# Performance work log

Measured on AMD Instinct MI355X. Metric: run time of the kernel, lower is better.

## Reference

```python
import jax, jax.numpy as jnp
import numpy as np

B, C, N, L, K, PRED = 64, 2, 1024, 24, 3, 12


def setup_inputs() -> dict:
    key = jax.random.key(0)
    ks = jax.random.split(key, 32)
    u = lambda k, shape, s: jax.random.uniform(k, shape, jnp.float32, -s, s)
    stdv_gc = 1.0 / np.sqrt(N)
    stdv_g = 1.0 / np.sqrt(N * (K + 1))
    stdv_r = 1.0 / np.sqrt(2 * N)
    inp = {
        'inputs': jax.random.normal(ks[0], (B, C, N, L), jnp.float32),
        'adj': (jax.random.uniform(ks[1], (N, N)) < 0.05).astype(jnp.float32),
        'gc_w': u(ks[2], (K, N, N), stdv_gc),
        'Wf': u(ks[3], (N, N * (K + 1)), stdv_g), 'bf': u(ks[4], (N,), stdv_g),
        'Wi': u(ks[5], (N, N * (K + 1)), stdv_g), 'bi': u(ks[6], (N,), stdv_g),
        'Wo': u(ks[7], (N, N * (K + 1)), stdv_g), 'bo': u(ks[8], (N,), stdv_g),
        'Wc': u(ks[9], (N, N * (K + 1)), stdv_g), 'bc': u(ks[10], (N,), stdv_g),
        'rWf': u(ks[11], (N, 2 * N), stdv_r), 'rbf': u(ks[12], (N,), stdv_r),
        'rWi': u(ks[13], (N, 2 * N), stdv_r), 'rbi': u(ks[14], (N,), stdv_r),
        'rWo': u(ks[15], (N, 2 * N), stdv_r), 'rbo': u(ks[16], (N,), stdv_r),
        'rWc': u(ks[17], (N, 2 * N), stdv_r), 'rbc': u(ks[18], (N,), stdv_r),
        'neighbor_w': u(ks[19], (N,), stdv_gc),
        'c': jnp.ones((1,), jnp.float32),
        'conv_w': u(ks[20], (C * PRED, C), 1.0 / np.sqrt(C)),
        'conv_b': u(ks[21], (C * PRED,), 1.0 / np.sqrt(C)),
    }
    return inp


def _build_A_list(adj, k):
    # tmp = sum(A, 0); zeros -> 1e-5; 'D_inverse' = diag(tmp) (as in original code)
    tmp = jnp.sum(adj, 0)
    tmp = jnp.where(tmp == 0, 1e-5, tmp)
    a_norm = tmp[:, None] * adj  # diag(tmp) @ A
    a_list = []
    a_tmp = jnp.eye(adj.shape[0], dtype=adj.dtype)
    for _ in range(k):
        a_tmp = jnp.minimum(a_tmp @ a_norm, 1.0)  # clamp max=1.0
        a_list.append(a_tmp)
    return a_list


def _forward(adj, inputs, gc_w, Wf, bf, Wi, bi, Wo, bo, Wc, bc,
             rWf, rbf, rWi, rbi, rWo, rbo, rWc, rbc, neighbor_w, c, conv_w, conv_b):
    b, ch, n, l = inputs.shape
    k = gc_w.shape[0]
    a_list = _build_A_list(adj, k)
    a_stack = jnp.stack(a_list)            # (K,N,N)
    eff_w = a_stack * gc_w                 # masked FilterLinear weights
    nbr = a_list[-1] @ neighbor_w          # (N,)
    Wg = jnp.concatenate([Wf, Wi, Wo, Wc], 0)      # fused gate weights (4N, (K+1)N)
    bg = jnp.concatenate([bf, bi, bo, bc], 0)
    rWg = jnp.concatenate([rWf, rWi, rWo, rWc], 0)  # (4N, 2N)
    rbg = jnp.concatenate([rbf, rbi, rbo, rbc], 0)

    def step(carry, x):  # x: (B,C,N)
        H, Cs, rH, rCs, _ = carry
        # gc = cat_k FilterLinear_k(x), each x @ (A_k*W_k)^T
        gc = jnp.einsum('bcn,kmn->bckm', x, eff_w).reshape(b, ch, k * n)
        g = jnp.concatenate([gc, H], -1) @ Wg.T + bg
        f, i, o, Ct = jnp.split(g, 4, -1)
        Cs = jax.nn.sigmoid(f) * (Cs * nbr) + jax.nn.sigmoid(i) * jnp.tanh(Ct)
        H = jax.nn.sigmoid(o) * jnp.tanh(Cs)
        rg = jnp.concatenate([x, rH], -1) @ rWg.T + rbg
        rf, ri, ro, rCt = jnp.split(rg, 4, -1)
        rCs = jax.nn.sigmoid(rf) * rCs + jax.nn.sigmoid(ri) * jnp.tanh(rCt)
        rH = jax.nn.sigmoid(ro) * jnp.tanh(rCs)
        var1 = jnp.var(x, axis=(0, 2), keepdims=True, ddof=1)   # (1,C,1), unbiased like torch
        var2 = jnp.var(gc, axis=(0, 2), keepdims=True, ddof=1)
        pred = (H * var1 * c + rH * var2) / (var1 + var2 * c)
        return (H, Cs, rH, rCs, pred), None

    z = jnp.zeros((b, ch, n), inputs.dtype)
    xs = jnp.moveaxis(inputs, -1, 0)  # (L,B,C,N)
    (H, Cs, rH, rCs, pred), _ = jax.lax.scan(step, (z, z, z, z, z), xs)
    # Conv1d(C, C*pred_len, k=1) then reshape (B,C,N,pred_len)
    out = jnp.einsum('bcn,oc->bon', pred, conv_w) + conv_b[:, None]
    return out.reshape(b, ch, n, -1)


def reference(inputs, adj, gc_w, Wf, bf, Wi, bi, Wo, bo, Wc, bc,
              rWf, rbf, rWi, rbi, rWo, rbo, rWc, rbc, neighbor_w, c, conv_w, conv_b):
    return _forward(adj, inputs, gc_w, Wf, bf, Wi, bi, Wo, bo, Wc, bc,
                    rWf, rbf, rWi, rbi, rWo, rbo, rWc, rbc, neighbor_w, c, conv_w, conv_b)
```

## Files before the change

### kernel.cpp

```cpp
#include <hip/hip_runtime.h>
#include <cmath>

#define NN 1024
#define BC 128
#define LS 24

typedef unsigned short u16;
typedef __attribute__((ext_vector_type(4))) float f32x4;
typedef __attribute__((ext_vector_type(8))) short bf16x8;
typedef __attribute__((ext_vector_type(8))) unsigned short u16x8;

typedef __attribute__((address_space(1))) const void* as1cv;
typedef __attribute__((address_space(3))) void* as3v;

#define GLD16(gp, lp) __builtin_amdgcn_global_load_lds((as1cv)(gp), (as3v)(lp), 16, 0, 0)

__device__ __forceinline__ float sigf(float x){ return 1.0f/(1.0f+expf(-x)); }

__device__ __forceinline__ u16 f2b(float x){
  union { float f; unsigned u; } v; v.f = x;
  unsigned r = v.u + 0x7FFFu + ((v.u >> 16) & 1u);
  return (u16)(r >> 16);
}
__device__ __forceinline__ float b2f(u16 b){
  union { unsigned u; float f; } v; v.u = ((unsigned)b) << 16;
  return v.f;
}

__global__ void k_prep(const float* __restrict__ inputs, const float* __restrict__ adj,
                       const float* __restrict__ Wf, const float* __restrict__ Wi,
                       const float* __restrict__ Wo, const float* __restrict__ Wc,
                       const float* __restrict__ rWf, const float* __restrict__ rWi,
                       const float* __restrict__ rWo, const float* __restrict__ rWc,
                       const float* __restrict__ bf_, const float* __restrict__ bi_,
                       const float* __restrict__ bo_, const float* __restrict__ bc_,
                       const float* __restrict__ rbf, const float* __restrict__ rbi,
                       const float* __restrict__ rbo, const float* __restrict__ rbc,
                       u16* __restrict__ Xb, float* __restrict__ csum,
                       u16* __restrict__ Wgxb, u16* __restrict__ WgHp,
                       u16* __restrict__ rWgxb, u16* __restrict__ rWgHp,
                       float* __restrict__ bgcat){
  int b = blockIdx.x, tid = threadIdx.x;
  if (b < 512){
    int idx = b*256 + tid;
    const float4* p = (const float4*)(inputs + (size_t)idx*LS);
    float v[LS];
    #pragma unroll
    for (int q = 0; q < 6; ++q){
      float4 f = p[q];
      v[q*4]=f.x; v[q*4+1]=f.y; v[q*4+2]=f.z; v[q*4+3]=f.w;
    }
    #pragma unroll
    for (int t = 0; t < LS; ++t)
      Xb[(size_t)t*BC*NN + idx] = f2b(v[t]);
  } else if (b < 576){
    int bb = b - 512;
    for (int j = tid; j < 1024; j += 256){
      float s = 0.f;
      for (int i = 0; i < 16; ++i) s += adj[(size_t)(bb*16+i)*1024 + j];
      csum[(size_t)bb*1024 + j] = s;
    }
  } else if (b < 592){
    int idx = (b-576)*256 + tid;
    int seg = idx >> 10, j = idx & 1023;
    bgcat[idx]      = (seg==0?bf_: seg==1?bi_: seg==2?bo_:bc_)[j];
    bgcat[4096+idx] = (seg==0?rbf: seg==1?rbi: seg==2?rbo:rbc)[j];
  } else {
    int idx = (b-592)*256 + tid;
    if (idx < 2097152){
      int kg = idx & 511, r = idx >> 9;
      int seg = r >> 10, j = r & 1023;
      const float* W = (seg==0?Wf: seg==1?Wi: seg==2?Wo:Wc) + (size_t)j*4096 + kg*8;
      float4 a = *(const float4*)W;
      float4 c = *(const float4*)(W + 4);
      u16x8 o = { f2b(a.x), f2b(a.y), f2b(a.z), f2b(a.w),
                  f2b(c.x), f2b(c.y), f2b(c.z), f2b(c.w) };
      if (kg < 384) *(u16x8*)(Wgxb + (size_t)r*3072 + kg*8) = o;
      else {
        int p = (j>>3)*32 + seg*8 + (j&7);
        *(u16x8*)(WgHp + (size_t)p*1024 + (kg*8 - 3072)) = o;
      }
    } else {
      int g2 = idx - 2097152;
      int kg = g2 & 255, r = g2 >> 8;
      int seg = r >> 10, j = r & 1023;
      const float* W = (seg==0?rWf: seg==1?rWi: seg==2?rWo:rWc) + (size_t)j*2048 + kg*8;
      float4 a = *(const float4*)W;
      float4 c = *(const float4*)(W + 4);
      u16x8 o = { f2b(a.x), f2b(a.y), f2b(a.z), f2b(a.w),
                  f2b(c.x), f2b(c.y), f2b(c.z), f2b(c.w) };
      if (kg < 128) *(u16x8*)(rWgxb + (size_t)r*1024 + kg*8) = o;
      else {
        int p = (j>>3)*32 + seg*8 + (j&7);
        *(u16x8*)(rWgHp + (size_t)p*1024 + (kg*8 - 1024)) = o;
      }
    }
  }
}

__global__ void k_colsum2(const float* __restrict__ part, float* __restrict__ tmp){
  int j = blockIdx.x*256 + threadIdx.x;
  float s = 0.f;
  for (int b = 0; b < 64; ++b) s += part[(size_t)b*1024 + j];
  tmp[j] = (s == 0.f) ? 1e-5f : s;
}

__global__ void k_anormT(const float* __restrict__ adj, const float* __restrict__ tmp,
                         u16* __restrict__ A1b, u16* __restrict__ anormT){
  __shared__ u16 t[64][65];
  int bi = blockIdx.y*64, bj = blockIdx.x*64;
  for (int e = threadIdx.x; e < 4096; e += 256){
    int r = e >> 6, cc = e & 63;
    float v = tmp[bi+r]*adj[(size_t)(bi+r)*1024 + bj+cc];
    A1b[(size_t)(bi+r)*1024 + bj+cc] = f2b(fminf(v, 1.f));
    t[r][cc] = f2b(v);
  }
  __syncthreads();
  for (int e = threadIdx.x; e < 4096; e += 256){
    int r = e >> 6, cc = e & 63;
    anormT[(size_t)(bj+r)*1024 + bi+cc] = t[cc][r];
  }
}

__global__ void k_nbr(const u16* __restrict__ A3b, const float* __restrict__ nw,
                      float* __restrict__ nbr){
  __shared__ float red[256];
  int row = blockIdx.x;
  float s = 0.f;
  for (int j = threadIdx.x; j < 1024; j += 256)
    s += b2f(A3b[(size_t)row*1024 + j])*nw[j];
  red[threadIdx.x] = s; __syncthreads();
  for (int st = 128; st > 0; st >>= 1){
    if (threadIdx.x < st) red[threadIdx.x] += red[threadIdx.x+st];
    __syncthreads();
  }
  if (threadIdx.x == 0) nbr[row] = red[0];
}

__global__ void k_effT(const u16* __restrict__ Ap, const float* __restrict__ gcw,
                       u16* __restrict__ effb, u16* __restrict__ effbT){
  __shared__ u16 t[64][65];
  int bi = blockIdx.y*64, bj = blockIdx.x*64;
  for (int e = threadIdx.x; e < 4096; e += 256){
    int r = e >> 6, cc = e & 63;
    size_t idx = (size_t)(bi+r)*1024 + bj+cc;
    u16 v = f2b(b2f(Ap[idx]) * gcw[idx]);
    effb[idx] = v;
    t[r][cc] = v;
  }
  __syncthreads();
  for (int e = threadIdx.x; e < 4096; e += 256){
    int r = e >> 6, cc = e & 63;
    effbT[(size_t)(bj+r)*3072 + bi+cc] = t[cc][r];
  }
}

__device__ __forceinline__ void mfma_tile(
    const u16* __restrict__ A, const u16* __restrict__ Bw, int K,
    const float* __restrict__ bias,
    float* __restrict__ outf, u16* __restrict__ outb, int ldc,
    u16* ldsA, u16* ldsB)
{
  const int tid  = threadIdx.x;
  const int lane = tid & 63;
  const int w    = tid >> 6;
  const int wr   = (w >> 1) * 64;
  const int wc   = (w & 1) * 64;
  f32x4 acc[4][4] = {};

  const int lrow = lane >> 3;
  const int srck = ((lane & 7) ^ lrow) * 8;
  for (int k0 = 0; k0 < K; k0 += 64){
    #pragma unroll
    for (int c = 0; c < 4; ++c){
      int row = w*32 + c*8;
      GLD16(A  + (size_t)(row + lrow)*K + k0 + srck, &ldsA[row*64]);
      GLD16(Bw + (size_t)(row + lrow)*K + k0 + srck, &ldsB[row*64]);
    }
    __syncthreads();
    #pragma unroll
    for (int kk = 0; kk < 2; ++kk) {
      bf16x8 af[4], bfr[4];
      #pragma unroll
      for (int mi = 0; mi < 4; ++mi) {
        int row = wr + mi*16 + (lane & 15);
        int grp = (kk*4 + (lane >> 4)) ^ (row & 7);
        af[mi] = *(const bf16x8*)&ldsA[row*64 + grp*8];
      }
      #pragma unroll
      for (int ni = 0; ni < 4; ++ni) {
        int row = wc + ni*16 + (lane & 15);
        int grp = (kk*4 + (lane >> 4)) ^ (row & 7);
        bfr[ni] = *(const bf16x8*)&ldsB[row*64 + grp*8];
      }
      #pragma unroll
      for (int mi = 0; mi < 4; ++mi)
        #pragma unroll
        for (int ni = 0; ni < 4; ++ni)
          acc[mi][ni] = __builtin_amdgcn_mfma_f32_16x16x32_bf16(af[mi], bfr[ni], acc[mi][ni], 0, 0, 0);
    }
    __syncthreads();
  }
  #pragma unroll
  for (int mi = 0; mi < 4; ++mi) {
    #pragma unroll
    for (int ni = 0; ni < 4; ++ni) {
      int col = wc + ni*16 + (lane & 15);
      #pragma unroll
      for (int q = 0; q < 4; ++q) {
        int row = wr + mi*16 + (lane >> 4)*4 + q;
        float v = acc[mi][ni][q];
        if (bias) v += bias[col];
        if (outf) outf[(size_t)row*ldc + col] = v;
        if (outb) outb[(size_t)row*ldc + col] = f2b(v);
      }
    }
  }
}

__global__ __launch_bounds__(256) void k_mfma_pre(
    const u16* __restrict__ Xb, const u16* __restrict__ Bcat,
    const float* __restrict__ bgcat, u16* __restrict__ prebuf)
{
  __shared__ u16 lds[16384];
  int id = blockIdx.y*64 + blockIdx.x;
  int bx = (id & 7)*8 + ((id >> 3) & 7);
  int by = id >> 6;
  mfma_tile(Xb + (size_t)by*128*1024, Bcat + (size_t)bx*128*1024, 1024,
            bgcat + bx*128, nullptr,
            prebuf + (size_t)by*128*8192 + bx*128, 8192,
            lds, lds + 8192);
}

__global__ __launch_bounds__(256) void k_mfma64(
    const u16* __restrict__ Ag, const u16* __restrict__ Bg, int K,
    int clamp1, int swz, u16* __restrict__ outb, int ldc)
{
  __shared__ u16 ldsA[64*128];
  __shared__ u16 ldsB[64*128];
  const int tid  = threadIdx.x;
  const int lane = tid & 63;
  const int w    = tid >> 6;
  const int wr   = (w >> 1) * 32;
  const int wc   = (w & 1) * 32;
  int bx = blockIdx.x, by = blockIdx.y;
  if (swz){
    int id = by*16 + bx;
    by = (id & 7)*8 + ((id >> 3) & 7);
    bx = id >> 6;
  }
  const u16* A = Ag + (size_t)by*64*K;
  const u16* B = Bg + (size_t)bx*64*K;
  f32x4 acc[2][2] = {};

  const int r4  = lane >> 4;
  const int g16 = lane & 15;
  for (int k0 = 0; k0 < K; k0 += 128){
    #pragma unroll
    for (int c = 0; c < 4; ++c){
      int rowb = w*16 + c*4;
      int row = rowb + r4;
      int srcg = (g16 & 8) | ((g16 & 7) ^ (row & 7));
      GLD16(A + (size_t)row*K + k0 + srcg*8, &ldsA[rowb*128]);
      GLD16(B + (size_t)row*K + k0 + srcg*8, &ldsB[rowb*128]);
    }
    __syncthreads();
    #pragma unroll
    for (int kk = 0; kk < 4; ++kk){
      int idx = kk*4 + (lane >> 4);
      bf16x8 af[2], bfr[2];
      #pragma unroll
      for (int mi = 0; mi < 2; ++mi){
        int row = wr + mi*16 + (lane & 15);
        int pa = (idx & 8) | ((idx & 7) ^ (row & 7));
        af[mi] = *(const bf16x8*)&ldsA[row*128 + pa*8];
      }
      #pragma unroll
      for (int ni = 0; ni < 2; ++ni){
        int row = wc + ni*16 + (lane & 15);
        int pb = (idx & 8) | ((idx & 7) ^ (row & 7));
        bfr[ni] = *(const bf16x8*)&ldsB[row*128 + pb*8];
      }
      #pragma unroll
      for (int mi = 0; mi < 2; ++mi)
        #pragma unroll
        for (int ni = 0; ni < 2; ++ni)
          acc[mi][ni] = __builtin_amdgcn_mfma_f32_16x16x32_bf16(af[mi], bfr[ni], acc[mi][ni], 0, 0, 0);
    }
    __syncthreads();
  }
  #pragma unroll
  for (int mi = 0; mi < 2; ++mi){
    #pragma unroll
    for (int ni = 0; ni < 2; ++ni){
      int col = bx*64 + wc + ni*16 + (lane & 15);
      #pragma unroll
      for (int q = 0; q < 4; ++q){
        int row = by*64 + wr + mi*16 + (lane >> 4)*4 + q;
        float v = acc[mi][ni][q];
        if (clamp1) v = fminf(v, 1.f);
        outb[(size_t)row*ldc + col] = f2b(v);
      }
    }
  }
}

__global__ __launch_bounds__(256) void k_step(
    const u16* __restrict__ WgHp, const u16* __restrict__ rWgHp,
    const u16* __restrict__ pre_t,
    const float* __restrict__ nbrv,
    u16* __restrict__ Hb2, u16* __restrict__ rHb2,
    float* __restrict__ Cs, float* __restrict__ rCs,
    float* __restrict__ Hf, float* __restrict__ rHf,
    int ph, int last)
{
  __shared__ u16 ldsA[64*256];
  __shared__ u16 ldsB[32*256];

  const int tid  = threadIdx.x;
  const int lane = tid & 63;
  const int w    = tid >> 6;
  const int bid  = blockIdx.x;
  const int job  = bid >> 8;
  const int rem  = bid & 255;
  const int s    = rem >> 1;
  const int r0   = (rem & 1) * 64;

  const u16* Bp   = (job ? rWgHp : WgHp) + (size_t)s*32*1024;
  const u16* Ab   = (job ? rHb2 : Hb2) + (size_t)ph*BC*NN + (size_t)r0*NN;
  const u16* pret = pre_t + (size_t)job*4096;
  u16* Hnext  = (job ? rHb2 : Hb2) + (size_t)(ph^1)*BC*NN;
  float* Csb  = job ? rCs : Cs;
  float* Hfin = job ? rHf : Hf;

  const int g32   = lane & 31;
  const int rhalf = lane >> 5;

  f32x4 acc[2] = {};
  for (int t = 0; t < 4; ++t){
    int k0 = t*256;
    #pragma unroll
    for (int c = 0; c < 8; ++c){
      int rowb = w*16 + c*2;
      int row = rowb + rhalf;
      int srcg = (g32 & 24) | ((g32 & 7) ^ (row & 7));
      GLD16(Ab + (size_t)row*1024 + k0 + srcg*8, &ldsA[rowb*256]);
    }
    #pragma unroll
    for (int c = 0; c < 4; ++c){
      int rowb = w*8 + c*2;
      int row = rowb + rhalf;
      int srcg = (g32 & 24) | ((g32 & 7) ^ (row & 7));
      GLD16(Bp + (size_t)row*1024 + k0 + srcg*8, &ldsB[rowb*256]);
    }
    __syncthreads();
    #pragma unroll
    for (int kk = 0; kk < 8; ++kk){
      int idx = kk*4 + (lane >> 4);
      int rowa = w*16 + (lane & 15);
      int pa = (idx & 24) | ((idx & 7) ^ (rowa & 7));
      bf16x8 af = *(const bf16x8*)&ldsA[rowa*256 + pa*8];
      #pragma unroll
      for (int ni = 0; ni < 2; ++ni){
        int rowb2 = ni*16 + (lane & 15);
        int pb = (idx & 24) | ((idx & 7) ^ (rowb2 & 7));
        bf16x8 bv = *(const bf16x8*)&ldsB[rowb2*256 + pb*8];
        acc[ni] = __builtin_amdgcn_mfma_f32_16x16x32_bf16(af, bv, acc[ni], 0, 0, 0);
      }
    }
    __syncthreads();
  }

  #pragma unroll
  for (int ni = 0; ni < 2; ++ni){
    int pcol = ni*16 + (lane & 15);
    int gcol = (pcol >> 3)*1024 + s*8 + (pcol & 7);
    #pragma unroll
    for (int q = 0; q < 4; ++q){
      int row = r0 + w*16 + (lane >> 4)*4 + q;
      acc[ni][q] += b2f(pret[(size_t)row*8192 + gcol]);
    }
  }
  const bool act = (lane & 15) < 8;
  const int  c   = lane & 7;
  const int  col = s*8 + c;
  float fac = 1.f;
  if (!job && act) fac = nbrv[col];
  #pragma unroll
  for (int q = 0; q < 4; ++q){
    float a0 = acc[0][q], a1 = acc[1][q];
    float p1 = __shfl_xor(a0, 8);
    float p3 = __shfl_xor(a1, 8);
    if (act){
      int row = r0 + w*16 + (lane >> 4)*4 + q;
      float fg = sigf(a0), ig = sigf(p1), og = sigf(a1), ct = tanhf(p3);
      size_t cidx = (size_t)row*NN + col;
      float cs = fg*Csb[cidx]*fac + ig*ct;
      Csb[cidx] = cs;
      float h = og*tanhf(cs);
      Hnext[cidx] = f2b(h);
      if (last) Hfin[cidx] = h;
    }
  }
}

__global__ void k_var1(const u16* __restrict__ Xl, const u16* __restrict__ gcl,
                       float* __restrict__ part){
  int ch = blockIdx.x & 1, seg = blockIdx.x >> 1;
  int tid = threadIdx.x;
  float s1=0.f,q1=0.f,s2=0.f,q2=0.f;
  for (int bb = 0; bb < 2; ++bb){
    int row = (seg*2+bb)*2 + ch;
    const u16* xr = Xl + (size_t)row*1024;
    for (int n = tid; n < 1024; n += 256){ float v = b2f(xr[n]); s1 += v; q1 += v*v; }
    const u16* gr = gcl + (size_t)row*3072;
    for (int n = tid; n < 3072; n += 256){ float v = b2f(gr[n]); s2 += v; q2 += v*v; }
  }
  __shared__ float red[256][4];
  red[tid][0]=s1; red[tid][1]=q1; red[tid][2]=s2; red[tid][3]=q2;
  __syncthreads();
  for (int st = 128; st > 0; st >>= 1){
    if (tid < st){ for (int z = 0; z < 4; ++z) red[tid][z] += red[tid+st][z]; }
    __syncthreads();
  }
  if (tid == 0){ for (int z = 0; z < 4; ++z) part[(size_t)blockIdx.x*4 + z] = red[0][z]; }
}

__global__ void k_out(const float* __restrict__ H, const float* __restrict__ rH,
                      const float* __restrict__ part, const float* __restrict__ cptr,
                      const float* __restrict__ cw, const float* __restrict__ cb,
                      float* __restrict__ out){
  __shared__ float vsh[4];
  int tid = threadIdx.x;
  if (tid < 4){
    int ch = tid & 1, which = tid >> 1;
    float s = 0.f, q = 0.f;
    for (int seg = 0; seg < 32; ++seg){
      const float* p = part + (size_t)(seg*2+ch)*4 + which*2;
      s += p[0]; q += p[1];
    }
    float n = which ? 196608.f : 65536.f;
    vsh[tid] = (q - s*s/n) / (n - 1.f);
  }
  __syncthreads();
  int idx = blockIdx.x*256 + tid;
  int n = idx & 1023, b = idx >> 10;
  float c0 = cptr[0];
  float v10 = vsh[0], v11 = vsh[1], v20 = vsh[2], v21 = vsh[3];
  size_t i0 = (size_t)(b*2+0)*1024 + n, i1 = (size_t)(b*2+1)*1024 + n;
  float p0 = (H[i0]*v10*c0 + rH[i0]*v20) / (v10 + v20*c0);
  float p1 = (H[i1]*v11*c0 + rH[i1]*v21) / (v11 + v21*c0);
  float* ob = out + (size_t)b*24*1024 + n;
  #pragma unroll
  for (int o = 0; o < 24; ++o)
    ob[(size_t)o*1024] = p0*cw[o*2+0] + p1*cw[o*2+1] + cb[o];
}

extern "C" void kernel_launch(void* const* d_in, const int* in_sizes, int n_in,
                              void* d_out, int out_size, void* d_ws, size_t ws_size,
                              hipStream_t stream) {
  const float* inputs = (const float*)d_in[0];
  const float* adj    = (const float*)d_in[1];
  const float* gcw    = (const float*)d_in[2];
  const float* Wf  = (const float*)d_in[3];  const float* bf_ = (const float*)d_in[4];
  const float* Wi  = (const float*)d_in[5];  const float* bi_ = (const float*)d_in[6];
  const float* Wo  = (const float*)d_in[7];  const float* bo_ = (const float*)d_in[8];
  const float* Wc  = (const float*)d_in[9];  const float* bc_ = (const float*)d_in[10];
  const float* rWf = (const float*)d_in[11]; const float* rbf = (const float*)d_in[12];
  const float* rWi = (const float*)d_in[13]; const float* rbi = (const float*)d_in[14];
  const float* rWo = (const float*)d_in[15]; const float* rbo = (const float*)d_in[16];
  const float* rWc = (const float*)d_in[17]; const float* rbc = (const float*)d_in[18];
  const float* nw     = (const float*)d_in[19];
  const float* cscal  = (const float*)d_in[20];
  const float* convw  = (const float*)d_in[21];
  const float* convb  = (const float*)d_in[22];
  float* out = (float*)d_out;

  char* cur = (char*)d_ws;
  auto alloc = [&](size_t bytes) -> void* {
    void* p = cur; cur += (bytes + 255) & ~(size_t)255; return p;
  };
  u16*   Xb     = (u16*)  alloc((size_t)LS*BC*NN*2);
  float* csum   = (float*)alloc((size_t)64*1024*4);
  float* tmpv   = (float*)alloc(1024*4);
  u16*   anormT = (u16*)  alloc((size_t)NN*NN*2);
  u16*   Apowb  = (u16*)  alloc((size_t)3*NN*NN*2);
  float* nbrv   = (float*)alloc(1024*4);
  u16*   effb   = (u16*)  alloc((size_t)3*NN*NN*2);
  u16*   effbT  = (u16*)  alloc((size_t)3*NN*NN*2);
  u16*   Wgxb   = (u16*)  alloc((size_t)4096*3072*2);
  u16*   WgHp   = (u16*)  alloc((size_t)4096*1024*2);
  u16*   rWgHp  = (u16*)  alloc((size_t)4096*1024*2);
  u16*   Bcat   = (u16*)  alloc((size_t)8192*1024*2);
  float* bgcat  = (float*)alloc(8192*4);
  u16*   gclb   = (u16*)  alloc((size_t)BC*3072*2);
  u16*   prebuf = (u16*)  alloc((size_t)3072*8192*2);
  char*  zbase  = cur;
  u16*   Hb2    = (u16*)  alloc((size_t)2*BC*NN*2);
  u16*   rHb2   = (u16*)  alloc((size_t)2*BC*NN*2);
  float* Cs     = (float*)alloc((size_t)BC*NN*4);
  float* rCs    = (float*)alloc((size_t)BC*NN*4);
  size_t zlen   = (size_t)(cur - zbase);
  float* Hfv    = (float*)alloc((size_t)BC*NN*4);
  float* rHfv   = (float*)alloc((size_t)BC*NN*4);
  float* part   = (float*)alloc(64*4*4);

  u16* A1b = Apowb;
  u16* A2b = Apowb + (size_t)NN*NN;
  u16* A3b = Apowb + (size_t)2*NN*NN;
  u16* Cwb   = Bcat;
  u16* rWgxb = Bcat + (size_t)4096*1024;

  k_prep<<<592 + (2097152+1048576)/256, 256, 0, stream>>>(
      inputs, adj, Wf, Wi, Wo, Wc, rWf, rWi, rWo, rWc,
      bf_, bi_, bo_, bc_, rbf, rbi, rbo, rbc,
      Xb, csum, Wgxb, WgHp, rWgxb, rWgHp, bgcat);
  k_colsum2<<<4, 256, 0, stream>>>(csum, tmpv);
  dim3 g16(16, 16);
  k_anormT<<<g16, 256, 0, stream>>>(adj, tmpv, A1b, anormT);
  k_mfma64<<<g16, 256, 0, stream>>>(A1b, anormT, 1024, 1, 0, A2b, 1024);
  k_mfma64<<<g16, 256, 0, stream>>>(A2b, anormT, 1024, 1, 0, A3b, 1024);
  k_nbr<<<NN, 256, 0, stream>>>(A3b, nw, nbrv);
  dim3 geff(16, 48);
  k_effT<<<geff, 256, 0, stream>>>(Apowb, gcw, effb, effbT);

  dim3 gcwg(16, 64);
  k_mfma64<<<gcwg, 256, 0, stream>>>(Wgxb, effbT, 3072, 0, 1, Cwb, 1024);
  dim3 gpre(64, 24);
  k_mfma_pre<<<gpre, 256, 0, stream>>>(Xb, Bcat, bgcat, prebuf);
  dim3 ggcl(48, 2);
  k_mfma64<<<ggcl, 256, 0, stream>>>(Xb + (size_t)(LS-1)*BC*NN, effb, 1024, 0, 0, gclb, 3072);

  hipMemsetAsync(zbase, 0, zlen, stream);

  for (int t = 0; t < LS; ++t)
    k_step<<<512, 256, 0, stream>>>(WgHp, rWgHp,
        prebuf + (size_t)t*BC*8192,
        nbrv, Hb2, rHb2, Cs, rCs, Hfv, rHfv, t & 1, t == LS-1);

  k_var1<<<64, 256, 0, stream>>>(Xb + (size_t)(LS-1)*BC*NN, gclb, part);
  k_out<<<(64*1024)/256, 256, 0, stream>>>(Hfv, rHfv, part, cscal, convw, convb, out);
}
```

Baseline: 529.6 us.

## Double-buffer LDS staging in recurrent step GEMM to overlap loads with MFMA

The k_step recurrent GEMM now splits K into 8 chunks of 128 with two LDS buffers, issuing global-to-LDS loads for the next chunk before computing the current one. It uses explicit vmcnt waits and raw s_barrier in place of __syncthreads. The goal is to hide global load latency behind MFMA work in this latency-bound per-timestep kernel. The cost is more barriers per chunk and reliance on hand-counted vmcnt values, which could break if the compiler changes how many loads it emits.

```diff
diff --git a/kernel.cpp b/kernel.cpp
--- a/kernel.cpp
+++ b/kernel.cpp
@@ -314,8 +314,8 @@
     float* __restrict__ Hf, float* __restrict__ rHf,
     int ph, int last)
 {
-  __shared__ u16 ldsA[64*256];
-  __shared__ u16 ldsB[32*256];
+  __shared__ u16 ldsA[2][64*128];
+  __shared__ u16 ldsB[2][32*128];
 
   const int tid  = threadIdx.x;
   const int lane = tid & 63;
@@ -333,42 +333,56 @@
   float* Csb  = job ? rCs : Cs;
   float* Hfin = job ? rHf : Hf;
 
-  const int g32   = lane & 31;
-  const int rhalf = lane >> 5;
+  const int r4  = lane >> 4;
+  const int g16 = lane & 15;
+
+  auto STAGE = [&](int ck, int buf){
+    int k0 = ck*128;
+    #pragma unroll
+    for (int c = 0; c < 4; ++c){
+      int rowb = w*16 + c*4;
+      int row = rowb + r4;
+      int srcg = (g16 & 8) | ((g16 & 7) ^ (row & 7));
+      GLD16(Ab + (size_t)row*1024 + k0 + srcg*8, &ldsA[buf][rowb*128]);
+    }
+    #pragma unroll
+    for (int c = 0; c < 2; ++c){
+      int rowb = w*8 + c*4;
+      int row = rowb + r4;
+      int srcg = (g16 & 8) | ((g16 & 7) ^ (row & 7));
+      GLD16(Bp + (size_t)row*1024 + k0 + srcg*8, &ldsB[buf][rowb*128]);
+    }
+  };
 
   f32x4 acc[2] = {};
-  for (int t = 0; t < 4; ++t){
-    int k0 = t*256;
-    #pragma unroll
-    for (int c = 0; c < 8; ++c){
-      int rowb = w*16 + c*2;
-      int row = rowb + rhalf;
-      int srcg = (g32 & 24) | ((g32 & 7) ^ (row & 7));
-      GLD16(Ab + (size_t)row*1024 + k0 + srcg*8, &ldsA[rowb*256]);
-    }
-    #pragma unroll
-    for (int c = 0; c < 4; ++c){
-      int rowb = w*8 + c*2;
-      int row = rowb + rhalf;
-      int srcg = (g32 & 24) | ((g32 & 7) ^ (row & 7));
-      GLD16(Bp + (size_t)row*1024 + k0 + srcg*8, &ldsB[rowb*256]);
-    }
-    __syncthreads();
-    #pragma unroll
-    for (int kk = 0; kk < 8; ++kk){
+  STAGE(0, 0);
+  #pragma unroll
+  for (int t = 0; t < 8; ++t){
+    const int cur = t & 1;
+    if (t < 7){
+      STAGE(t+1, cur^1);
+      asm volatile("s_waitcnt vmcnt(6)" ::: "memory");
+    } else {
+      asm volatile("s_waitcnt vmcnt(0)" ::: "memory");
+    }
+    __builtin_amdgcn_sched_barrier(0);
+    __builtin_amdgcn_s_barrier();
+    #pragma unroll
+    for (int kk = 0; kk < 4; ++kk){
       int idx = kk*4 + (lane >> 4);
       int rowa = w*16 + (lane & 15);
-      int pa = (idx & 24) | ((idx & 7) ^ (rowa & 7));
-      bf16x8 af = *(const bf16x8*)&ldsA[rowa*256 + pa*8];
+      int pa = (idx & 8) | ((idx & 7) ^ (rowa & 7));
+      bf16x8 af = *(const bf16x8*)&ldsA[cur][rowa*128 + pa*8];
       #pragma unroll
       for (int ni = 0; ni < 2; ++ni){
         int rowb2 = ni*16 + (lane & 15);
-        int pb = (idx & 24) | ((idx & 7) ^ (rowb2 & 7));
-        bf16x8 bv = *(const bf16x8*)&ldsB[rowb2*256 + pb*8];
+        int pb = (idx & 8) | ((idx & 7) ^ (rowb2 & 7));
+        bf16x8 bv = *(const bf16x8*)&ldsB[cur][rowb2*128 + pb*8];
         acc[ni] = __builtin_amdgcn_mfma_f32_16x16x32_bf16(af, bv, acc[ni], 0, 0, 0);
       }
     }
-    __syncthreads();
+    __builtin_amdgcn_sched_barrier(0);
+    __builtin_amdgcn_s_barrier();
   }
 
   #pragma unroll
```

Measured after the change: 529.3 us. About the same (-0.0%).
